# Kernel tuning notes

Hardware: AMD Instinct MI355X
Metric: run time of the kernel (lower is better)

## Reference

```python
import jax, jax.numpy as jnp
import numpy as np
import math

N, E, D, H = 1536, 49152, 512, 8
DH = D // H  # head dim = 64
SCALE = 256.0 * math.sqrt(2.0)  # rel_dists scaling in forward


def sinusoidal_pe(x, d):
    """x: [...] float positions -> [..., d] interleaved sin/cos encoding."""
    div = jnp.exp(jnp.arange(0, d, 2, dtype=jnp.float32) * (-math.log(10000.0) / d))
    ang = x[..., None] * div  # [..., d//2]
    return jnp.stack([jnp.sin(ang), jnp.cos(ang)], axis=-1).reshape(*x.shape, d)


def setup_inputs() -> dict:
    key = jax.random.key(0)
    ks = jax.random.split(key, 8)
    features = jax.random.normal(ks[0], (N, D), dtype=jnp.float32)
    edge_index = jax.random.randint(ks[1], (2, E), 0, N, dtype=jnp.int64)
    edge_attr = jax.random.uniform(ks[2], (E,), dtype=jnp.float32)  # normalized distances
    pos = jax.random.uniform(ks[3], (N, 2), dtype=jnp.float32)  # unused by forward
    s = 1.0 / math.sqrt(D)  # ~xavier-uniform bound sqrt(6/(D+D))... use simple symmetric init
    Wq = jax.random.uniform(ks[4], (D, D), minval=-s, maxval=s, dtype=jnp.float32)
    Wk = jax.random.uniform(ks[5], (D, D), minval=-s, maxval=s, dtype=jnp.float32)
    Wv = jax.random.uniform(ks[6], (D, D), minval=-s, maxval=s, dtype=jnp.float32)
    bq = jnp.zeros((D,), jnp.float32)
    bk = jnp.zeros((D,), jnp.float32)
    bv = jnp.zeros((D,), jnp.float32)
    return dict(features=features, edge_index=edge_index, edge_attr=edge_attr, pos=pos,
                Wq=Wq, bq=bq, Wk=Wk, bk=bk, Wv=Wv, bv=bv)


def reference(features, edge_index, edge_attr, pos, Wq, bq, Wk, bk, Wv, bv):
    # batch dim is 1 in the original (features.unsqueeze(0)); we omit it.
    q = (features @ Wq.T + bq).reshape(N, H, DH).transpose(1, 0, 2)  # [H,N,DH]
    k = (features @ Wk.T + bk).reshape(N, H, DH).transpose(1, 0, 2)
    v = (features @ Wv.T + bv).reshape(N, H, DH).transpose(1, 0, 2)

    qk = jnp.einsum('hqd,hrd->hqr', q, k)  # [H,N,N]

    # to_dense_adj: scatter-add edge_attr into dense [N,N], then scale
    rel = jnp.zeros((N, N), jnp.float32).at[edge_index[0], edge_index[1]].add(edge_attr) * SCALE
    # embed_k and embed_q are identical parameter-free sinusoidal encodings of rel
    rk = sinusoidal_pe(rel, DH)  # [N,N,DH]

    # original: qk + q.rk + k.rq + (q_repeat*k_repeat == qk)  => 2*qk + q.rk + k.rk
    logits = 2.0 * qk \
        + jnp.einsum('hqd,qrd->hqr', q, rk) \
        + jnp.einsum('hrd,qrd->hqr', k, rk)
    attn = jax.nn.softmax(logits / math.sqrt(DH), axis=-1)  # [H,N,N]

    out = jnp.einsum('hqr,hrd->hqd', attn, v)  # [H,N,DH]
    out = out.transpose(1, 0, 2).reshape(N, D)  # [N,D]
    return out.max(axis=0)  # [D] max-pool over nodes (MIL pooling)
```

## Files before the change

kernel.cpp:

```cpp
#include <hip/hip_runtime.h>
#include <cmath>


constexpr int Nn  = 1536;
constexpr int Dd  = 512;
constexpr int Hh  = 8;
constexpr int DHd = 64;
constexpr int SPLITS = 4;
constexpr float SCALE_F = 362.03867196751236f;
constexpr float M0 = 8.0f;

typedef float f4 __attribute__((ext_vector_type(4)));
typedef int   i4 __attribute__((ext_vector_type(4)));
typedef __attribute__((ext_vector_type(4))) float f32x4;
typedef __attribute__((ext_vector_type(8))) short bf16x8;

__device__ inline unsigned short bf16_rne(float x) {
    unsigned u = __float_as_uint(x);
    unsigned r = u + 0x7fff + ((u >> 16) & 1);
    return (unsigned short)(r >> 16);
}
__device__ inline float bf16_tof(unsigned short h) {
    return __uint_as_float(((unsigned)h) << 16);
}

__global__ __launch_bounds__(256) void pack_fw_k(
    const float* __restrict__ feat,
    const float* __restrict__ Wq, const float* __restrict__ Wk, const float* __restrict__ Wv,
    unsigned short* __restrict__ pFh, unsigned short* __restrict__ pFl,
    unsigned short* __restrict__ pWh, unsigned short* __restrict__ pWl)
{
    int tg = blockIdx.x * 256 + threadIdx.x;
    int type = blockIdx.y;
    int L = tg & 63;
    int kc = (tg >> 6) & 15;
    int t10 = tg >> 10;
    const float* src;
    unsigned short *oh, *ol;
    int row, col;
    if (type == 0) {
        src = feat; oh = pFh; ol = pFl;
        row = t10 * 16 + (L & 15);
        col = kc * 32 + (L >> 4) * 8;
    } else {
        int z = t10 >> 5, nt = t10 & 31;
        src = (z == 0) ? Wq : (z == 1) ? Wk : Wv;
        oh = pWh; ol = pWl;
        row = nt * 16 + (L & 15);
        col = kc * 32 + (L >> 4) * 8;
    }
    f4 a = *(const f4*)(src + (size_t)row * Dd + col);
    f4 b = *(const f4*)(src + (size_t)row * Dd + col + 4);
    float x[8];
    #pragma unroll
    for (int j = 0; j < 4; ++j) { x[j] = a[j]; x[4 + j] = b[j]; }
    unsigned short hs[8], ls[8];
    #pragma unroll
    for (int j = 0; j < 8; ++j) {
        hs[j] = bf16_rne(x[j]);
        ls[j] = bf16_rne(x[j] - bf16_tof(hs[j]));
    }
    *(bf16x8*)(oh + (size_t)tg * 8) = *(bf16x8*)hs;
    *(bf16x8*)(ol + (size_t)tg * 8) = *(bf16x8*)ls;
}

__global__ __launch_bounds__(256) void qkvm_k(
    const unsigned short* __restrict__ pFh, const unsigned short* __restrict__ pFl,
    const unsigned short* __restrict__ pWh, const unsigned short* __restrict__ pWl,
    const float* __restrict__ bq, const float* __restrict__ bk, const float* __restrict__ bv,
    float* __restrict__ Qo, float* __restrict__ Ko, float* __restrict__ Vo)
{
    const int z = blockIdx.z;
    const float* __restrict__ bias = (z == 0) ? bq : (z == 1) ? bk : bv;
    float* __restrict__ outp       = (z == 0) ? Qo : (z == 1) ? Ko : Vo;
    const int tid = threadIdx.x;
    const int L = tid & 63, wv = tid >> 6;
    const int l15 = L & 15, quad = L >> 4;
    const int mt0 = blockIdx.y * 4 + (wv & 1) * 2;
    const int nt0 = blockIdx.x * 4 + (wv >> 1) * 2;

    f32x4 acc[2][2];
    #pragma unroll
    for (int i = 0; i < 2; ++i)
        #pragma unroll
        for (int j = 0; j < 2; ++j) acc[i][j] = (f32x4){0.f, 0.f, 0.f, 0.f};

    for (int kc = 0; kc < 16; ++kc) {
        bf16x8 ah[2], al[2], bh[2], bl[2];
        #pragma unroll
        for (int i = 0; i < 2; ++i) {
            size_t ao = ((size_t)((mt0 + i) * 16 + kc)) * 512 + L * 8;
            ah[i] = *(const bf16x8*)(pFh + ao);
            al[i] = *(const bf16x8*)(pFl + ao);
            size_t bo = ((size_t)((z * 32 + nt0 + i) * 16 + kc)) * 512 + L * 8;
            bh[i] = *(const bf16x8*)(pWh + bo);
            bl[i] = *(const bf16x8*)(pWl + bo);
        }
        #pragma unroll
        for (int i = 0; i < 2; ++i)
            #pragma unroll
            for (int j = 0; j < 2; ++j) {
                f32x4 a = acc[i][j];
                a = __builtin_amdgcn_mfma_f32_16x16x32_bf16(ah[i], bh[j], a, 0, 0, 0);
                a = __builtin_amdgcn_mfma_f32_16x16x32_bf16(ah[i], bl[j], a, 0, 0, 0);
                a = __builtin_amdgcn_mfma_f32_16x16x32_bf16(al[i], bh[j], a, 0, 0, 0);
                a = __builtin_amdgcn_mfma_f32_16x16x32_bf16(al[i], bl[j], a, 0, 0, 0);
                acc[i][j] = a;
            }
    }

    #pragma unroll
    for (int i = 0; i < 2; ++i) {
        int row0 = (mt0 + i) * 16 + quad * 4;
        #pragma unroll
        for (int j = 0; j < 2; ++j) {
            int col = (nt0 + j) * 16 + l15;
            float b = bias[col];
            #pragma unroll
            for (int reg = 0; reg < 4; ++reg)
                outp[(size_t)(row0 + reg) * Dd + col] = acc[i][j][reg] + b;
        }
    }
}

__global__ __launch_bounds__(256) void pack_k(
    const float* __restrict__ Q, const float* __restrict__ K, const float* __restrict__ V,
    unsigned short* __restrict__ pQh, unsigned short* __restrict__ pQl,
    unsigned short* __restrict__ pKh, unsigned short* __restrict__ pKl,
    unsigned short* __restrict__ pVh, unsigned short* __restrict__ pVl)
{
    int tg = blockIdx.x * 256 + threadIdx.x;
    int type = blockIdx.y;
    int L = tg & 63;
    float x[8];
    unsigned short* oh;
    unsigned short* ol;
    if (type < 2) {
        const float* src = type ? K : Q;
        oh = type ? pKh : pQh;
        ol = type ? pKl : pQl;
        int kc = (tg >> 6) & 1;
        int mt = (tg >> 7) % 96;
        int h  = (tg >> 7) / 96;
        int row = mt * 16 + (L & 15);
        int col = h * 64 + kc * 32 + (L >> 4) * 8;
        f4 a = *(const f4*)(src + (size_t)row * Dd + col);
        f4 b = *(const f4*)(src + (size_t)row * Dd + col + 4);
        float sc = type ? 1.0f : 0.25f;
        #pragma unroll
        for (int j = 0; j < 4; ++j) { x[j] = a[j] * sc; x[4 + j] = b[j] * sc; }
    } else {
        oh = pVh; ol = pVl;
        int dt = (tg >> 6) & 3;
        int rc = (tg >> 8) % 48;
        int h  = (tg >> 8) / 48;
        int col  = h * 64 + dt * 16 + (L & 15);
        int row0 = rc * 32 + (L >> 4) * 8;
        #pragma unroll
        for (int j = 0; j < 8; ++j) x[j] = V[(size_t)(row0 + j) * Dd + col];
    }
    unsigned short hs[8], ls[8];
    #pragma unroll
    for (int j = 0; j < 8; ++j) {
        hs[j] = bf16_rne(x[j]);
        ls[j] = bf16_rne(x[j] - bf16_tof(hs[j]));
    }
    *(bf16x8*)(oh + (size_t)tg * 8) = *(bf16x8*)hs;
    *(bf16x8*)(ol + (size_t)tg * 8) = *(bf16x8*)ls;
}

__global__ __launch_bounds__(256) void init_rel_k(float* __restrict__ rel, int* __restrict__ eid)
{
    size_t i = ((size_t)blockIdx.x * 256 + threadIdx.x) * 4;
    if (i < (size_t)Nn * Nn) {
        *(f4*)(rel + i) = (f4){0.f, 0.f, 0.f, 0.f};
        *(i4*)(eid + i) = (i4){-1, -1, -1, -1};
    }
}

__global__ __launch_bounds__(256) void scatter_k(
    const int* __restrict__ raw, const float* __restrict__ attr,
    float* __restrict__ rel, int* __restrict__ eid, int* __restrict__ idxn, int E)
{
    int e = blockIdx.x * 256 + threadIdx.x;
    if (e >= E) return;
    int acc = 0;
    #pragma unroll
    for (int i = 0; i < 16; ++i) acc |= raw[2 * i + 1];
    int s, t;
    if (acc == 0) { s = raw[2 * e]; t = raw[2 * (E + e)]; }
    else          { s = raw[e];     t = raw[E + e]; }
    idxn[e] = s; idxn[E + e] = t;
    size_t off = (size_t)s * Nn + t;
    atomicAdd(rel + off, attr[e] * SCALE_F);
    eid[off] = e;
}

__global__ void oddsum_k(const float* __restrict__ Q, const float* __restrict__ K,
                         float* __restrict__ qodd, float* __restrict__ kodd,
                         float* __restrict__ koddT)
{
    int t = blockIdx.x * 256 + threadIdx.x;
    if (t >= 2 * Nn * Hh) return;
    const float* src = (t < Nn * Hh) ? Q : K;
    int i = (t < Nn * Hh) ? t : t - Nn * Hh;
    int n = i >> 3, h = i & 7;
    const float* row = src + (size_t)n * Dd + h * DHd;
    float s = 0.f;
    #pragma unroll
    for (int ii = 0; ii < 32; ++ii) s += row[2 * ii + 1];
    if (t < Nn * Hh) qodd[i] = s;
    else { kodd[i] = s; koddT[h * Nn + n] = 0.125f * s; }
}

__global__ __launch_bounds__(256) void delta_k(
    const int* __restrict__ idxn, const float* __restrict__ rel,
    const float* __restrict__ Q, const float* __restrict__ K,
    const float* __restrict__ qodd, const float* __restrict__ kodd,
    float* __restrict__ delta8, int E)
{
    int t = blockIdx.x * 256 + threadIdx.x;
    if (t >= E * Hh) return;
    int e = t >> 3, h = t & 7;
    int qi = idxn[e], ri = idxn[E + e];
    float x = rel[(size_t)qi * Nn + ri];
    const float* qrow = Q + (size_t)qi * Dd + h * DHd;
    const float* krow = K + (size_t)ri * Dd + h * DHd;
    float acc = 0.f;
    #pragma unroll
    for (int i = 0; i < 32; i += 2) {
        float d0 = expf(-0.28782313662425572f * (float)i);
        float d1 = expf(-0.28782313662425572f * (float)(i + 1));
        float s0, c0, s1, c1;
        __sincosf(x * d0, &s0, &c0);
        __sincosf(x * d1, &s1, &c1);
        f4 q4 = *(const f4*)(qrow + 2 * i);
        f4 k4 = *(const f4*)(krow + 2 * i);
        acc += (q4[0] + k4[0]) * s0 + (q4[1] + k4[1]) * c0
             + (q4[2] + k4[2]) * s1 + (q4[3] + k4[3]) * c1;
    }
    delta8[(size_t)e * Hh + h] = 0.125f * (acc - qodd[qi * Hh + h] - kodd[ri * Hh + h]);
}

__global__ __launch_bounds__(64, 3) void flash5_k(
    const unsigned short* __restrict__ pQh, const unsigned short* __restrict__ pQl,
    const unsigned short* __restrict__ pKh, const unsigned short* __restrict__ pKl,
    const unsigned short* __restrict__ pVh, const unsigned short* __restrict__ pVl,
    const int* __restrict__ eid, const float* __restrict__ delta8,
    const float* __restrict__ koddT,
    float* __restrict__ Opart, float* __restrict__ Lpart)
{
    const int qt = blockIdx.x, h = blockIdx.y, s = blockIdx.z;
    const int L = threadIdx.x, quad = L >> 4, l15 = L & 15;
    const int q0 = qt * 16;
    __shared__ unsigned short phi[16][80];
    __shared__ unsigned short plo[16][80];

    bf16x8 qh[2], ql[2];
    #pragma unroll
    for (int kc = 0; kc < 2; ++kc) {
        size_t off = ((size_t)((h * 96 + qt) * 2 + kc)) * 512 + L * 8;
        qh[kc] = *(const bf16x8*)(pQh + off);
        ql[kc] = *(const bf16x8*)(pQl + off);
    }

    f32x4 O[4];
    float lsum[4];
    #pragma unroll
    for (int r = 0; r < 4; ++r) { lsum[r] = 0.f; O[r] = (f32x4){0.f, 0.f, 0.f, 0.f}; }

    const int NT = 24 / SPLITS;
    const int Tbase = s * NT;

    bf16x8 kh0[4], kh1[4], kl0[4], kl1[4];
    {
        const int r0 = Tbase * 64;
        #pragma unroll
        for (int nt = 0; nt < 4; ++nt) {
            size_t b0 = ((size_t)((h * 96 + (r0 >> 4) + nt) * 2)) * 512 + L * 8;
            kh0[nt] = *(const bf16x8*)(pKh + b0);
            kh1[nt] = *(const bf16x8*)(pKh + b0 + 512);
            kl0[nt] = *(const bf16x8*)(pKl + b0);
            kl1[nt] = *(const bf16x8*)(pKl + b0 + 512);
        }
    }

    float kvcur[4], dcur[16];
    {
        const int r0 = Tbase * 64;
        int ecur[16];
        #pragma unroll
        for (int nt = 0; nt < 4; ++nt) {
            kvcur[nt] = koddT[h * Nn + r0 + nt * 16 + l15];
            #pragma unroll
            for (int reg = 0; reg < 4; ++reg)
                ecur[nt * 4 + reg] = eid[(size_t)(q0 + quad * 4 + reg) * Nn + r0 + nt * 16 + l15];
        }
        #pragma unroll
        for (int i = 0; i < 16; ++i) {
            int e = ecur[i];
            float d = delta8[(size_t)(e < 0 ? 0 : e) * Hh + h];
            dcur[i] = (e >= 0) ? d : 0.f;
        }
    }

    for (int T = 0; T < NT; ++T) {
        const int r0 = (Tbase + T) * 64;
        const bool more = (T + 1 < NT);

        int   enxt[16];
        float kvnxt[4];
        if (more) {
            const int r1 = r0 + 64;
            #pragma unroll
            for (int nt = 0; nt < 4; ++nt) {
                kvnxt[nt] = koddT[h * Nn + r1 + nt * 16 + l15];
                #pragma unroll
                for (int reg = 0; reg < 4; ++reg)
                    enxt[nt * 4 + reg] = eid[(size_t)(q0 + quad * 4 + reg) * Nn + r1 + nt * 16 + l15];
            }
        }

        bf16x8 vh0[4], vh1[4], vl0[4], vl1[4];
        #pragma unroll
        for (int dt = 0; dt < 4; ++dt) {
            size_t vb = ((size_t)((h * 48 + (r0 >> 5)) * 4 + dt)) * 512 + L * 8;
            vh0[dt] = *(const bf16x8*)(pVh + vb);
            vh1[dt] = *(const bf16x8*)(pVh + vb + 2048);
            vl0[dt] = *(const bf16x8*)(pVl + vb);
            vl1[dt] = *(const bf16x8*)(pVl + vb + 2048);
        }

        f32x4 S[4];
        #pragma unroll
        for (int nt = 0; nt < 4; ++nt) {
            f32x4 a = {0.f, 0.f, 0.f, 0.f};
            a = __builtin_amdgcn_mfma_f32_16x16x32_bf16(qh[0], kh0[nt], a, 0, 0, 0);
            a = __builtin_amdgcn_mfma_f32_16x16x32_bf16(qh[1], kh1[nt], a, 0, 0, 0);
            a = __builtin_amdgcn_mfma_f32_16x16x32_bf16(qh[0], kl0[nt], a, 0, 0, 0);
            a = __builtin_amdgcn_mfma_f32_16x16x32_bf16(qh[1], kl1[nt], a, 0, 0, 0);
            a = __builtin_amdgcn_mfma_f32_16x16x32_bf16(ql[0], kh0[nt], a, 0, 0, 0);
            a = __builtin_amdgcn_mfma_f32_16x16x32_bf16(ql[1], kh1[nt], a, 0, 0, 0);
            S[nt] = a;
        }

        if (more) {
            const int r1 = r0 + 64;
            #pragma unroll
            for (int nt = 0; nt < 4; ++nt) {
                size_t b0 = ((size_t)((h * 96 + (r1 >> 4) + nt) * 2)) * 512 + L * 8;
                kh0[nt] = *(const bf16x8*)(pKh + b0);
                kh1[nt] = *(const bf16x8*)(pKh + b0 + 512);
                kl0[nt] = *(const bf16x8*)(pKl + b0);
                kl1[nt] = *(const bf16x8*)(pKl + b0 + 512);
            }
        }

        #pragma unroll
        for (int reg = 0; reg < 4; ++reg) {
            float p[4];
            #pragma unroll
            for (int nt = 0; nt < 4; ++nt) {
                p[nt] = __expf(S[nt][reg] + kvcur[nt] + dcur[nt * 4 + reg] - M0);
                lsum[reg] += p[nt];
                unsigned short hi = bf16_rne(p[nt]);
                phi[quad * 4 + reg][nt * 16 + l15] = hi;
                plo[quad * 4 + reg][nt * 16 + l15] = bf16_rne(p[nt] - bf16_tof(hi));
            }
        }

        bf16x8 ph[2], pl[2];
        #pragma unroll
        for (int kc2 = 0; kc2 < 2; ++kc2) {
            ph[kc2] = *(const bf16x8*)&phi[l15][kc2 * 32 + quad * 8];
            pl[kc2] = *(const bf16x8*)&plo[l15][kc2 * 32 + quad * 8];
        }

        #pragma unroll
        for (int dt = 0; dt < 4; ++dt) {
            f32x4 a = O[dt];
            a = __builtin_amdgcn_mfma_f32_16x16x32_bf16(ph[0], vh0[dt], a, 0, 0, 0);
            a = __builtin_amdgcn_mfma_f32_16x16x32_bf16(ph[1], vh1[dt], a, 0, 0, 0);
            a = __builtin_amdgcn_mfma_f32_16x16x32_bf16(ph[0], vl0[dt], a, 0, 0, 0);
            a = __builtin_amdgcn_mfma_f32_16x16x32_bf16(ph[1], vl1[dt], a, 0, 0, 0);
            a = __builtin_amdgcn_mfma_f32_16x16x32_bf16(pl[0], vh0[dt], a, 0, 0, 0);
            a = __builtin_amdgcn_mfma_f32_16x16x32_bf16(pl[1], vh1[dt], a, 0, 0, 0);
            O[dt] = a;
        }

        if (more) {
            #pragma unroll
            for (int i = 0; i < 16; ++i) {
                int e = enxt[i];
                float d = delta8[(size_t)(e < 0 ? 0 : e) * Hh + h];
                dcur[i] = (e >= 0) ? d : 0.f;
            }
            #pragma unroll
            for (int nt = 0; nt < 4; ++nt) kvcur[nt] = kvnxt[nt];
        }
    }

    #pragma unroll
    for (int reg = 0; reg < 4; ++reg) {
        #pragma unroll
        for (int o = 1; o < 16; o <<= 1) lsum[reg] += __shfl_xor(lsum[reg], o);
    }

    #pragma unroll
    for (int dt = 0; dt < 4; ++dt)
        #pragma unroll
        for (int reg = 0; reg < 4; ++reg)
            Opart[((size_t)(s * Hh + h) * Nn + q0 + quad * 4 + reg) * 64 + dt * 16 + l15] = O[dt][reg];
    if (l15 == 0) {
        #pragma unroll
        for (int reg = 0; reg < 4; ++reg)
            Lpart[(size_t)(s * Hh + h) * Nn + q0 + quad * 4 + reg] = lsum[reg];
    }
}

__global__ __launch_bounds__(256) void combine_mp_k(
    const float* __restrict__ Opart, const float* __restrict__ Lpart,
    float* __restrict__ partial)
{
    const int b = blockIdx.x;
    const int t = threadIdx.x;
    const int cg = (t & 127) * 4;
    const int h = cg >> 6, d = cg & 63;
    const int rh = t >> 7;
    f4 mx = {-3.0e38f, -3.0e38f, -3.0e38f, -3.0e38f};
    for (int r = 0; r < 8; ++r) {
        int q = b * 16 + rh * 8 + r;
        float l = 0.f;
        f4 o = {0.f, 0.f, 0.f, 0.f};
        #pragma unroll
        for (int s2 = 0; s2 < SPLITS; ++s2) {
            l += Lpart[(size_t)(s2 * Hh + h) * Nn + q];
            f4 ov = *(const f4*)(Opart + ((size_t)(s2 * Hh + h) * Nn + q) * 64 + d);
            #pragma unroll
            for (int c = 0; c < 4; ++c) o[c] += ov[c];
        }
        float inv = 1.0f / l;
        #pragma unroll
        for (int c = 0; c < 4; ++c) mx[c] = fmaxf(mx[c], o[c] * inv);
    }
    *(f4*)(partial + (size_t)(b * 2 + rh) * 512 + cg) = mx;
}

__global__ __launch_bounds__(128) void mp2_k(const float* __restrict__ partial,
                                             float* __restrict__ outp)
{
    const int t = threadIdx.x;
    f4 mx = {-3.0e38f, -3.0e38f, -3.0e38f, -3.0e38f};
    for (int b = 0; b < 192; ++b) {
        f4 v = *(const f4*)(partial + (size_t)b * 512 + 4 * t);
        #pragma unroll
        for (int c = 0; c < 4; ++c) mx[c] = fmaxf(mx[c], v[c]);
    }
    *(f4*)(outp + 4 * t) = mx;
}

extern "C" void kernel_launch(void* const* d_in, const int* in_sizes, int n_in,
                              void* d_out, int out_size, void* d_ws, size_t ws_size,
                              hipStream_t stream)
{
    const float* feat   = (const float*)d_in[0];
    const int*   rawidx = (const int*)d_in[1];
    const float* attr   = (const float*)d_in[2];
    const float* Wq = (const float*)d_in[4];
    const float* bq = (const float*)d_in[5];
    const float* Wk = (const float*)d_in[6];
    const float* bk = (const float*)d_in[7];
    const float* Wv = (const float*)d_in[8];
    const float* bv = (const float*)d_in[9];
    float* outp = (float*)d_out;
    const int E = in_sizes[2];

    const size_t ND_ = (size_t)Nn * Dd;
    const size_t NN_ = (size_t)Nn * Nn;
    const size_t PK_ = (size_t)Hh * 96 * 2 * 512;
    float* ws    = (float*)d_ws;
    float* Q     = ws;
    float* K     = Q + ND_;
    float* V     = K + ND_;
    float* rel   = V + ND_;
    int*   eid   = (int*)(rel + NN_);
    float* delta8 = (float*)(eid + NN_);
    float* qodd  = delta8 + (size_t)E * Hh;
    float* kodd  = qodd + (size_t)Nn * Hh;
    float* koddT = kodd + (size_t)Nn * Hh;
    int*   idxn  = (int*)(koddT + (size_t)Nn * Hh);
    unsigned short* pQh = (unsigned short*)(idxn + 2 * E);
    unsigned short* pQl = pQh + PK_;
    unsigned short* pKh = pQl + PK_;
    unsigned short* pKl = pKh + PK_;
    unsigned short* pVh = pKl + PK_;
    unsigned short* pVl = pVh + PK_;
    float* Lpart = (float*)(pVl + PK_);
    float* partial = Lpart + (size_t)SPLITS * Hh * Nn;
    unsigned short* pFh = (unsigned short*)(partial + 192 * 512);
    unsigned short* pFl = pFh + PK_;
    unsigned short* pWh = pFl + PK_;
    unsigned short* pWl = pWh + PK_;
    float* Opart = ws;

    pack_fw_k<<<dim3(384, 2), 256, 0, stream>>>(feat, Wq, Wk, Wv, pFh, pFl, pWh, pWl);
    qkvm_k<<<dim3(8, 24, 3), 256, 0, stream>>>(pFh, pFl, pWh, pWl, bq, bk, bv, Q, K, V);
    init_rel_k<<<(int)((NN_ / 4 + 255) / 256), 256, 0, stream>>>(rel, eid);
    scatter_k<<<(E + 255) / 256, 256, 0, stream>>>(rawidx, attr, rel, eid, idxn, E);
    oddsum_k<<<(2 * Nn * Hh + 255) / 256, 256, 0, stream>>>(Q, K, qodd, kodd, koddT);
    delta_k<<<(E * Hh + 255) / 256, 256, 0, stream>>>(idxn, rel, Q, K, qodd, kodd, delta8, E);
    pack_k<<<dim3(384, 3), 256, 0, stream>>>(Q, K, V, pQh, pQl, pKh, pKl, pVh, pVl);
    flash5_k<<<dim3(96, 8, SPLITS), 64, 0, stream>>>(pQh, pQl, pKh, pKl, pVh, pVl,
                                                     eid, delta8, koddT, Opart, Lpart);
    combine_mp_k<<<96, 256, 0, stream>>>(Opart, Lpart, partial);
    mp2_k<<<1, 128, 0, stream>>>(partial, outp);
}
```

Baseline: 193.5 us.

## Raise flash splits and occupancy, pipeline QKV loads, atomic max-pool, cheaper sincos

```diff
diff --git a/kernel.cpp b/kernel.cpp
--- a/kernel.cpp
+++ b/kernel.cpp
@@ -6,7 +6,7 @@
 constexpr int Dd  = 512;
 constexpr int Hh  = 8;
 constexpr int DHd = 64;
-constexpr int SPLITS = 4;
+constexpr int SPLITS = 6;
 constexpr float SCALE_F = 362.03867196751236f;
 constexpr float M0 = 8.0f;
 
@@ -22,6 +22,10 @@
 }
 __device__ inline float bf16_tof(unsigned short h) {
     return __uint_as_float(((unsigned)h) << 16);
+}
+__device__ inline unsigned f2ord(float x) {
+    unsigned b = __float_as_uint(x);
+    return (b & 0x80000000u) ? ~b : (b | 0x80000000u);
 }
 
 __global__ __launch_bounds__(256) void pack_fw_k(
@@ -85,28 +89,39 @@
         #pragma unroll
         for (int j = 0; j < 2; ++j) acc[i][j] = (f32x4){0.f, 0.f, 0.f, 0.f};
 
-    for (int kc = 0; kc < 16; ++kc) {
-        bf16x8 ah[2], al[2], bh[2], bl[2];
+    bf16x8 AH[2][2], AL[2][2], BH[2][2], BL[2][2];
+    auto loadset = [&](int buf, int kc) {
         #pragma unroll
         for (int i = 0; i < 2; ++i) {
             size_t ao = ((size_t)((mt0 + i) * 16 + kc)) * 512 + L * 8;
-            ah[i] = *(const bf16x8*)(pFh + ao);
-            al[i] = *(const bf16x8*)(pFl + ao);
+            AH[buf][i] = *(const bf16x8*)(pFh + ao);
+            AL[buf][i] = *(const bf16x8*)(pFl + ao);
             size_t bo = ((size_t)((z * 32 + nt0 + i) * 16 + kc)) * 512 + L * 8;
-            bh[i] = *(const bf16x8*)(pWh + bo);
-            bl[i] = *(const bf16x8*)(pWl + bo);
-        }
+            BH[buf][i] = *(const bf16x8*)(pWh + bo);
+            BL[buf][i] = *(const bf16x8*)(pWl + bo);
+        }
+    };
+    auto mfmaset = [&](int buf) {
         #pragma unroll
         for (int i = 0; i < 2; ++i)
             #pragma unroll
             for (int j = 0; j < 2; ++j) {
                 f32x4 a = acc[i][j];
-                a = __builtin_amdgcn_mfma_f32_16x16x32_bf16(ah[i], bh[j], a, 0, 0, 0);
-                a = __builtin_amdgcn_mfma_f32_16x16x32_bf16(ah[i], bl[j], a, 0, 0, 0);
-                a = __builtin_amdgcn_mfma_f32_16x16x32_bf16(al[i], bh[j], a, 0, 0, 0);
-                a = __builtin_amdgcn_mfma_f32_16x16x32_bf16(al[i], bl[j], a, 0, 0, 0);
+                a = __builtin_amdgcn_mfma_f32_16x16x32_bf16(AH[buf][i], BH[buf][j], a, 0, 0, 0);
+                a = __builtin_amdgcn_mfma_f32_16x16x32_bf16(AH[buf][i], BL[buf][j], a, 0, 0, 0);
+                a = __builtin_amdgcn_mfma_f32_16x16x32_bf16(AL[buf][i], BH[buf][j], a, 0, 0, 0);
+                a = __builtin_amdgcn_mfma_f32_16x16x32_bf16(AL[buf][i], BL[buf][j], a, 0, 0, 0);
                 acc[i][j] = a;
             }
+    };
+
+    loadset(0, 0);
+    #pragma unroll
+    for (int kc = 0; kc < 16; kc += 2) {
+        loadset(1, kc + 1);
+        mfmaset(0);
+        if (kc + 2 < 16) loadset(0, kc + 2);
+        mfmaset(1);
     }
 
     #pragma unroll
@@ -169,12 +184,19 @@
     *(bf16x8*)(ol + (size_t)tg * 8) = *(bf16x8*)ls;
 }
 
-__global__ __launch_bounds__(256) void init_rel_k(float* __restrict__ rel, int* __restrict__ eid)
-{
-    size_t i = ((size_t)blockIdx.x * 256 + threadIdx.x) * 4;
+__global__ __launch_bounds__(256) void init_rel_k(float* __restrict__ rel,
+                                                  int* __restrict__ eid,
+                                                  unsigned* __restrict__ ordmax)
+{
+    size_t idx = (size_t)blockIdx.x * 256 + threadIdx.x;
+    size_t i = idx * 4;
     if (i < (size_t)Nn * Nn) {
         *(f4*)(rel + i) = (f4){0.f, 0.f, 0.f, 0.f};
         *(i4*)(eid + i) = (i4){-1, -1, -1, -1};
+    }
+    if (idx < 128) {
+        #pragma unroll
+        for (int c = 0; c < 4; ++c) ordmax[idx * 4 + c] = 0x007FFFFFu;
     }
 }
 
@@ -229,11 +251,12 @@
     float acc = 0.f;
     #pragma unroll
     for (int i = 0; i < 32; i += 2) {
-        float d0 = expf(-0.28782313662425572f * (float)i);
-        float d1 = expf(-0.28782313662425572f * (float)(i + 1));
-        float s0, c0, s1, c1;
-        __sincosf(x * d0, &s0, &c0);
-        __sincosf(x * d1, &s1, &c1);
+        float dd0 = 0.15915494309189535f * __builtin_amdgcn_exp2f(-0.4152410118609203f * (float)i);
+        float dd1 = 0.15915494309189535f * __builtin_amdgcn_exp2f(-0.4152410118609203f * (float)(i + 1));
+        float r0 = x * dd0; r0 -= floorf(r0);
+        float r1 = x * dd1; r1 -= floorf(r1);
+        float s0 = __builtin_amdgcn_sinf(r0), c0 = __builtin_amdgcn_cosf(r0);
+        float s1 = __builtin_amdgcn_sinf(r1), c1 = __builtin_amdgcn_cosf(r1);
         f4 q4 = *(const f4*)(qrow + 2 * i);
         f4 k4 = *(const f4*)(krow + 2 * i);
         acc += (q4[0] + k4[0]) * s0 + (q4[1] + k4[1]) * c0
@@ -242,7 +265,7 @@
     delta8[(size_t)e * Hh + h] = 0.125f * (acc - qodd[qi * Hh + h] - kodd[ri * Hh + h]);
 }
 
-__global__ __launch_bounds__(64, 3) void flash5_k(
+__global__ __launch_bounds__(64, 4) void flash6_k(
     const unsigned short* __restrict__ pQh, const unsigned short* __restrict__ pQl,
     const unsigned short* __restrict__ pKh, const unsigned short* __restrict__ pKl,
     const unsigned short* __restrict__ pVh, const unsigned short* __restrict__ pVl,
@@ -420,7 +443,7 @@
 
 __global__ __launch_bounds__(256) void combine_mp_k(
     const float* __restrict__ Opart, const float* __restrict__ Lpart,
-    float* __restrict__ partial)
+    unsigned* __restrict__ ordmax)
 {
     const int b = blockIdx.x;
     const int t = threadIdx.x;
@@ -443,20 +466,16 @@
         #pragma unroll
         for (int c = 0; c < 4; ++c) mx[c] = fmaxf(mx[c], o[c] * inv);
     }
-    *(f4*)(partial + (size_t)(b * 2 + rh) * 512 + cg) = mx;
-}
-
-__global__ __launch_bounds__(128) void mp2_k(const float* __restrict__ partial,
-                                             float* __restrict__ outp)
-{
-    const int t = threadIdx.x;
-    f4 mx = {-3.0e38f, -3.0e38f, -3.0e38f, -3.0e38f};
-    for (int b = 0; b < 192; ++b) {
-        f4 v = *(const f4*)(partial + (size_t)b * 512 + 4 * t);
-        #pragma unroll
-        for (int c = 0; c < 4; ++c) mx[c] = fmaxf(mx[c], v[c]);
-    }
-    *(f4*)(outp + 4 * t) = mx;
+    #pragma unroll
+    for (int c = 0; c < 4; ++c) atomicMax(&ordmax[cg + c], f2ord(mx[c]));
+}
+
+__global__ void decode_k(const unsigned* __restrict__ ordmax, float* __restrict__ outp)
+{
+    int t = blockIdx.x * 256 + threadIdx.x;
+    if (t >= Dd) return;
+    unsigned u = ordmax[t];
+    outp[t] = (u & 0x80000000u) ? __uint_as_float(u ^ 0x80000000u) : __uint_as_float(~u);
 }
 
 extern "C" void kernel_launch(void* const* d_in, const int* in_sizes, int n_in,
@@ -482,7 +501,11 @@
     float* Q     = ws;
     float* K     = Q + ND_;
     float* V     = K + ND_;
-    float* rel   = V + ND_;
+    unsigned short* pFh = (unsigned short*)(V + ND_);
+    unsigned short* pFl = pFh + PK_;
+    unsigned short* pWh = pFl + PK_;
+    unsigned short* pWl = pWh + PK_;
+    float* rel   = (float*)(pWl + PK_);
     int*   eid   = (int*)(rel + NN_);
     float* delta8 = (float*)(eid + NN_);
     float* qodd  = delta8 + (size_t)E * Hh;
@@ -496,22 +519,18 @@
     unsigned short* pVh = pKl + PK_;
     unsigned short* pVl = pVh + PK_;
     float* Lpart = (float*)(pVl + PK_);
-    float* partial = Lpart + (size_t)SPLITS * Hh * Nn;
-    unsigned short* pFh = (unsigned short*)(partial + 192 * 512);
-    unsigned short* pFl = pFh + PK_;
-    unsigned short* pWh = pFl + PK_;
-    unsigned short* pWl = pWh + PK_;
+    unsigned* ordmax = (unsigned*)(Lpart + (size_t)SPLITS * Hh * Nn);
     float* Opart = ws;
 
     pack_fw_k<<<dim3(384, 2), 256, 0, stream>>>(feat, Wq, Wk, Wv, pFh, pFl, pWh, pWl);
     qkvm_k<<<dim3(8, 24, 3), 256, 0, stream>>>(pFh, pFl, pWh, pWl, bq, bk, bv, Q, K, V);
-    init_rel_k<<<(int)((NN_ / 4 + 255) / 256), 256, 0, stream>>>(rel, eid);
+    init_rel_k<<<(int)((NN_ / 4 + 255) / 256), 256, 0, stream>>>(rel, eid, ordmax);
     scatter_k<<<(E + 255) / 256, 256, 0, stream>>>(rawidx, attr, rel, eid, idxn, E);
     oddsum_k<<<(2 * Nn * Hh + 255) / 256, 256, 0, stream>>>(Q, K, qodd, kodd, koddT);
     delta_k<<<(E * Hh + 255) / 256, 256, 0, stream>>>(idxn, rel, Q, K, qodd, kodd, delta8, E);
     pack_k<<<dim3(384, 3), 256, 0, stream>>>(Q, K, V, pQh, pQl, pKh, pKl, pVh, pVl);
-    flash5_k<<<dim3(96, 8, SPLITS), 64, 0, stream>>>(pQh, pQl, pKh, pKl, pVh, pVl,
+    flash6_k<<<dim3(96, 8, SPLITS), 64, 0, stream>>>(pQh, pQl, pKh, pKl, pVh, pVl,
                                                      eid, delta8, koddT, Opart, Lpart);
-    combine_mp_k<<<96, 256, 0, stream>>>(Opart, Lpart, partial);
-    mp2_k<<<1, 128, 0, stream>>>(partial, outp);
-}
+    combine_mp_k<<<96, 256, 0, stream>>>(Opart, Lpart, ordmax);
+    decode_k<<<(Dd + 255) / 256, 256, 0, stream>>>(ordmax, outp);
+}
```

New measurement: 221.2 us. 1.14x slower.
